# Kernel optimization log

Measured on AMD Instinct MI355X. Metric: run time of the kernel, lower is better.

The kernel has to match this reference:

```python
import jax, jax.numpy as jnp
import numpy as np

N_LAYER, N_HEAD, D_PARAM = 4, 8, 63
BATCH, SEQ, D_FULL = 16, 2048, D_PARAM + 1
VAR = 0.02


def setup_inputs() -> dict:
    key = jax.random.key(0)
    kz, kp = jax.random.split(key)
    Z = jax.random.normal(kz, (BATCH, SEQ, D_FULL), dtype=jnp.float32)
    allparam = VAR * jax.random.normal(kp, (N_LAYER, N_HEAD, 2, D_PARAM, D_PARAM), dtype=jnp.float32)
    return {"Z": Z, "allparam": allparam}


def _augment(P, Q, d_full):
    # P_full: P in top-left block, bottom-right corner = 1, rest zeros.
    dp = P.shape[0]
    P_full = jnp.zeros((d_full, d_full), P.dtype).at[:dp, :dp].set(P).at[dp, dp].set(1.0)
    # Q_full: Q in top-left block, rest zeros (bottom-right corner stays 0).
    Q_full = jnp.zeros((d_full, d_full), Q.dtype).at[:dp, :dp].set(Q)
    return P_full, Q_full


def _attention(P, Q, Z):
    B, N, d = Z.shape
    P_full, Q_full = _augment(P, Q, d)
    # attn[b,n,m] = Z[b,n,:] @ Q_full @ Z[b,m,:]
    attn = jnp.einsum('BNi,ij,BMj->BNM', Z, Q_full, Z)
    key = jnp.einsum('ij,BNj->BNi', P_full, Z)
    # A = eye(N) with A[N-1,N-1] = 0  => zero out last token of key before aggregation.
    key = key.at[:, N - 1, :].set(0.0)
    out = jnp.einsum('BNM,BMi->BNi', attn, key)
    return out / (N - 1)


def reference(Z, allparam):
    n_layer, n_head = allparam.shape[0], allparam.shape[1]
    for i in range(n_layer):
        Zi = Z
        residues = jnp.zeros_like(Z)
        for j in range(n_head):
            residues = residues + _attention(allparam[i, j, 0], allparam[i, j, 1], Zi)
        Z = Zi + residues
    return Z
```

## Files before the change

kernel.cpp:

```cpp
#include <hip/hip_runtime.h>
#include <hip/hip_bf16.h>

constexpr int NL = 4;
constexpr int NH = 8;
constexpr int DP = 63;
constexpr int D  = 64;
constexpr int B  = 16;
constexpr int S  = 2048;
constexpr int CHUNKS = 16;
constexpr int ROWS_PER_CHUNK = S / CHUNKS;

__global__ __launch_bounds__(256) void kA(const float* __restrict__ Z,
                                          float* __restrict__ Gp) {
    const int b = blockIdx.x;
    const int c = blockIdx.y;
    __shared__ float lz[64][64];
    const int t   = threadIdx.x;
    const int col = t & 63;
    const int rb  = t >> 6;

    float acc[16];
#pragma unroll
    for (int k = 0; k < 16; ++k) acc[k] = 0.f;

    const int rowbase = c * ROWS_PER_CHUNK;
    for (int sub = 0; sub < ROWS_PER_CHUNK / 64; ++sub) {
#pragma unroll
        for (int k = 0; k < 16; ++k) {
            int row  = rb + 4 * k;
            int grow = rowbase + sub * 64 + row;
            float v  = Z[((size_t)b * S + grow) * D + col];
            if (grow == S - 1) v = 0.f;
            lz[row][col] = v;
        }
        __syncthreads();
        for (int m = 0; m < 64; ++m) {
            float zr = lz[m][col];
#pragma unroll
            for (int k = 0; k < 16; ++k)
                acc[k] += lz[m][rb + 4 * k] * zr;
        }
        __syncthreads();
    }
    float* outp = Gp + ((size_t)(c * B + b)) * (D * D);
#pragma unroll
    for (int k = 0; k < 16; ++k)
        outp[(rb + 4 * k) * D + col] = acc[k];
}

__global__ __launch_bounds__(256) void kB(const float* __restrict__ Gp,
                                          const float* __restrict__ allparam,
                                          float* __restrict__ H, int layer) {
    const int b = blockIdx.x;
    const int j = blockIdx.y;
    __shared__ float G[64 * 64];
    __shared__ float PfT[64 * 64];
    __shared__ float Qf[64 * 64];
    __shared__ float T[64 * 64];

    const int t   = threadIdx.x;
    const int col = t & 63;
    const int rb  = t >> 6;

#pragma unroll
    for (int k = 0; k < 16; ++k) {
        int e = t + 256 * k;
        float s = 0.f;
        for (int c2 = 0; c2 < CHUNKS; ++c2)
            s += Gp[((size_t)(c2 * B + b)) * (D * D) + e];
        G[e] = s;
    }

    const float* P = allparam + ((size_t)((layer * NH + j) * 2 + 0)) * (DP * DP);
    const float* Q = allparam + ((size_t)((layer * NH + j) * 2 + 1)) * (DP * DP);
#pragma unroll
    for (int k = 0; k < 16; ++k) {
        int e = t + 256 * k;
        int r = e >> 6, i = e & 63;
        float pv = 0.f;
        if (r < DP && i < DP) pv = P[i * DP + r];
        if (r == DP && i == DP) pv = 1.f;
        PfT[e] = pv;
        int p = r, q = i;
        Qf[e] = (p < DP && q < DP) ? Q[p * DP + q] : 0.f;
    }
    __syncthreads();

    {
        float acc[16];
#pragma unroll
        for (int k = 0; k < 16; ++k) acc[k] = 0.f;
        for (int r = 0; r < 64; ++r) {
            float pv = PfT[r * 64 + col];
#pragma unroll
            for (int k = 0; k < 16; ++k)
                acc[k] += G[(rb + 4 * k) * 64 + r] * pv;
        }
#pragma unroll
        for (int k = 0; k < 16; ++k)
            T[(rb + 4 * k) * 64 + col] = acc[k];
    }
    __syncthreads();

    {
        const float inv = 1.0f / (float)(S - 1);
        float acc[16];
#pragma unroll
        for (int k = 0; k < 16; ++k) acc[k] = 0.f;
        for (int q = 0; q < 64; ++q) {
            float tv = T[q * 64 + col];
#pragma unroll
            for (int k = 0; k < 16; ++k)
                acc[k] += Qf[(rb + 4 * k) * 64 + q] * tv;
        }
        float* Hout = H + ((size_t)(b * NH + j)) * (D * D);
#pragma unroll
        for (int k = 0; k < 16; ++k)
            Hout[(rb + 4 * k) * 64 + col] = acc[k] * inv;
    }
}

__global__ __launch_bounds__(256) void kB2(const float* __restrict__ H,
                                           float* __restrict__ W) {
    const int b = blockIdx.x;
    const int t = threadIdx.x;
#pragma unroll
    for (int k = 0; k < 16; ++k) {
        int e = t + 256 * k;
        float s = ((e >> 6) == (e & 63)) ? 1.f : 0.f;
        for (int j = 0; j < NH; ++j)
            s += H[((size_t)(b * NH + j)) * (D * D) + e];
        W[(size_t)b * (D * D) + e] = s;
    }
}

__global__ __launch_bounds__(256) void kC(const float* Zin,
                                          const float* __restrict__ W,
                                          float* Zout) {
    const int b    = blockIdx.x;
    const int tile = blockIdx.y;
    __shared__ float lz[64][64];
    __shared__ float lw[64][64];
    const int t   = threadIdx.x;
    const int col = t & 63;
    const int rb  = t >> 6;

#pragma unroll
    for (int k = 0; k < 16; ++k) {
        int e = t + 256 * k;
        lw[e >> 6][e & 63] = W[(size_t)b * (D * D) + e];
    }
    const size_t zbase = ((size_t)b * S + (size_t)tile * 64) * D;
#pragma unroll
    for (int k = 0; k < 16; ++k) {
        int row = rb + 4 * k;
        lz[row][col] = Zin[zbase + (size_t)row * D + col];
    }
    __syncthreads();

    float acc[16];
#pragma unroll
    for (int k = 0; k < 16; ++k) acc[k] = 0.f;
    for (int p = 0; p < 64; ++p) {
        float wv = lw[p][col];
#pragma unroll
        for (int k = 0; k < 16; ++k)
            acc[k] += lz[rb + 4 * k][p] * wv;
    }
#pragma unroll
    for (int k = 0; k < 16; ++k) {
        int row = rb + 4 * k;
        Zout[zbase + (size_t)row * D + col] = acc[k];
    }
}

extern "C" void kernel_launch(void* const* d_in, const int* in_sizes, int n_in,
                              void* d_out, int out_size, void* d_ws, size_t ws_size,
                              hipStream_t stream) {
    const float* Z        = (const float*)d_in[0];
    const float* allparam = (const float*)d_in[1];
    float* out = (float*)d_out;

    float* Gp = (float*)d_ws;
    float* H  = Gp + (size_t)CHUNKS * B * (D * D);
    float* W  = H + (size_t)B * NH * (D * D);

    for (int layer = 0; layer < NL; ++layer) {
        const float* src = (layer == 0) ? Z : (const float*)out;
        kA <<<dim3(B, CHUNKS), 256, 0, stream>>>(src, Gp);
        kB <<<dim3(B, NH),     256, 0, stream>>>(Gp, allparam, H, layer);
        kB2<<<B,               256, 0, stream>>>(H, W);
        kC <<<dim3(B, S / 64), 256, 0, stream>>>(src, W, out);
    }
}
```

Measured before the change: 225.2 us.

## Fuse next-layer Gram into Z update, register-tile GEMMs, atomic head accumulation

Replaces the per-layer four-kernel pipeline with a first Gram kernel plus, per layer, a reduce kernel, a weight kernel and an update kernel. The update kernel also computes the next layer's partial Gram from the freshly computed tile, so Z is not re-read. The GEMMs now use 8x8 and 4x4 register tiles with float4 loads and XOR-swizzled shared memory. Head contributions go into W through atomicAdd instead of a separate sum kernel. Atomics make the float summation order nondeterministic, and the larger shared-memory use may lower occupancy.

New measurement: 210.5 us. 6.6% less time.

```diff
diff --git a/kernel.cpp b/kernel.cpp
--- a/kernel.cpp
+++ b/kernel.cpp
@@ -1,177 +1,213 @@
 #include <hip/hip_runtime.h>
-#include <hip/hip_bf16.h>
-
-constexpr int NL = 4;
-constexpr int NH = 8;
-constexpr int DP = 63;
-constexpr int D  = 64;
-constexpr int B  = 16;
-constexpr int S  = 2048;
-constexpr int CHUNKS = 16;
-constexpr int ROWS_PER_CHUNK = S / CHUNKS;
-
-__global__ __launch_bounds__(256) void kA(const float* __restrict__ Z,
-                                          float* __restrict__ Gp) {
-    const int b = blockIdx.x;
-    const int c = blockIdx.y;
-    __shared__ float lz[64][64];
-    const int t   = threadIdx.x;
-    const int col = t & 63;
-    const int rb  = t >> 6;
-
-    float acc[16];
-#pragma unroll
-    for (int k = 0; k < 16; ++k) acc[k] = 0.f;
-
-    const int rowbase = c * ROWS_PER_CHUNK;
-    for (int sub = 0; sub < ROWS_PER_CHUNK / 64; ++sub) {
-#pragma unroll
-        for (int k = 0; k < 16; ++k) {
-            int row  = rb + 4 * k;
-            int grow = rowbase + sub * 64 + row;
-            float v  = Z[((size_t)b * S + grow) * D + col];
-            if (grow == S - 1) v = 0.f;
-            lz[row][col] = v;
+
+constexpr int NH = 8, DP = 63, D = 64, B = 16, S = 2048;
+constexpr int TILE = 128, NTILE = 16;
+constexpr float INVS = 1.0f / 2047.0f;
+
+__device__ __forceinline__ void gram_reduce_store(const float* ZN, float4* sm4,
+                                                  float* __restrict__ gp, int t) {
+    const int w = t >> 6, l = t & 63, qy = l >> 3, rx = l & 7;
+    float g[8][8];
+#pragma unroll
+    for (int a = 0; a < 8; ++a)
+#pragma unroll
+        for (int bb = 0; bb < 8; ++bb) g[a][bb] = 0.f;
+
+#pragma unroll 4
+    for (int mi = 0; mi < 32; ++mi) {
+        const int m = 32 * w + mi;
+        const int f = (m >> 3) & 15;
+        const float* rowp = &ZN[m * 64];
+        float4 a0 = *(const float4*)&rowp[4 * (qy ^ f)];
+        float4 a1 = *(const float4*)&rowp[4 * ((qy + 8) ^ f)];
+        float4 b0 = *(const float4*)&rowp[4 * (rx ^ f)];
+        float4 b1 = *(const float4*)&rowp[4 * ((rx + 8) ^ f)];
+        float A[8]  = {a0.x, a0.y, a0.z, a0.w, a1.x, a1.y, a1.z, a1.w};
+        float Bv[8] = {b0.x, b0.y, b0.z, b0.w, b1.x, b1.y, b1.z, b1.w};
+#pragma unroll
+        for (int a = 0; a < 8; ++a)
+#pragma unroll
+            for (int bb = 0; bb < 8; ++bb) g[a][bb] += A[a] * Bv[bb];
+    }
+    __syncthreads();
+
+    float* part = (float*)(sm4 + w * 1024);
+#pragma unroll
+    for (int a = 0; a < 8; ++a) {
+        const int q = 4 * qy + (a & 3) + 32 * (a >> 2);
+        *(float4*)&part[q * 64 + 4 * rx]      = make_float4(g[a][0], g[a][1], g[a][2], g[a][3]);
+        *(float4*)&part[q * 64 + 32 + 4 * rx] = make_float4(g[a][4], g[a][5], g[a][6], g[a][7]);
+    }
+    __syncthreads();
+
+    float4* gp4 = (float4*)gp;
+#pragma unroll
+    for (int k = 0; k < 4; ++k) {
+        const int e4 = t + 256 * k;
+        float4 s0 = sm4[e4], s1 = sm4[1024 + e4], s2 = sm4[2048 + e4], s3 = sm4[3072 + e4];
+        gp4[e4] = make_float4(s0.x + s1.x + s2.x + s3.x, s0.y + s1.y + s2.y + s3.y,
+                              s0.z + s1.z + s2.z + s3.z, s0.w + s1.w + s2.w + s3.w);
+    }
+}
+
+__global__ __launch_bounds__(256) void kGram0(const float* __restrict__ Z,
+                                              float* __restrict__ Gp) {
+    __shared__ float4 sm4[5120];
+    float* ZN = (float*)(sm4 + 3072);
+    const int b = blockIdx.x, tile = blockIdx.y, t = threadIdx.x;
+#pragma unroll
+    for (int k = 0; k < 8; ++k) {
+        const int row = (t >> 4) + 16 * k, c4 = t & 15;
+        const int grow = tile * TILE + row;
+        float4 v = *(const float4*)&Z[((size_t)b * S + grow) * D + 4 * c4];
+        if (grow == S - 1) v = make_float4(0.f, 0.f, 0.f, 0.f);
+        *(float4*)&ZN[row * 64 + 4 * (c4 ^ ((row >> 3) & 15))] = v;
+    }
+    __syncthreads();
+    gram_reduce_store(ZN, sm4, Gp + ((size_t)(b * 16 + tile)) * 4096, t);
+}
+
+__global__ __launch_bounds__(256) void kRed(const float* __restrict__ Gp,
+                                            float* __restrict__ G,
+                                            float* __restrict__ W) {
+    const int b = blockIdx.x, s = blockIdx.y, t = threadIdx.x;
+    const int e = s * 256 + t;
+    float sum = 0.f;
+#pragma unroll 4
+    for (int p = 0; p < 16; ++p) sum += Gp[((size_t)(b * 16 + p)) * 4096 + e];
+    G[(size_t)b * 4096 + e] = sum;
+    W[(size_t)b * 4096 + e] = ((e >> 6) == (e & 63)) ? 1.f : 0.f;
+}
+
+__global__ __launch_bounds__(128) void kW(const float* __restrict__ G,
+                                          const float* __restrict__ params,
+                                          float* __restrict__ W) {
+    __shared__ float4 sm4[(4096 + 2048 + 4096 + 2048) / 4];
+    float* Gs = (float*)sm4;
+    float* Pt = Gs + 4096;
+    float* Qt = Pt + 2048;
+    float* T  = Qt + 4096;
+    const int b = blockIdx.x, j = blockIdx.y, s = blockIdx.z, t = threadIdx.x;
+    const int ty = t >> 3, tx = t & 7;
+    const float* P = params + (size_t)(j * 2 + 0) * (DP * DP);
+    const float* Q = params + (size_t)(j * 2 + 1) * (DP * DP);
+
+#pragma unroll
+    for (int k = 0; k < 8; ++k)
+        ((float4*)Gs)[t + 128 * k] = ((const float4*)(G + (size_t)b * 4096))[t + 128 * k];
+#pragma unroll
+    for (int k = 0; k < 16; ++k) {
+        const int r = t & 63, ii = (t >> 6) + 2 * k;
+        const int i = 32 * s + ii;
+        float v = 0.f;
+        if (r < DP && i < DP) v = P[(size_t)i * DP + r];
+        else if (r == DP && i == DP) v = 1.f;
+        Pt[r * 32 + 4 * ((ii >> 2) ^ (r & 7)) + (ii & 3)] = v;
+    }
+#pragma unroll
+    for (int k = 0; k < 32; ++k) {
+        const int q = t & 63, p = (t >> 6) + 2 * k;
+        const float v = (p < DP && q < DP) ? Q[(size_t)p * DP + q] : 0.f;
+        Qt[q * 64 + 4 * ((p >> 2) ^ (q & 15)) + (p & 3)] = v;
+    }
+    __syncthreads();
+
+    float acc[4][4] = {};
+#pragma unroll 4
+    for (int r = 0; r < 64; ++r) {
+        float4 av = *(const float4*)&Gs[r * 64 + 4 * ty];
+        float4 bv = *(const float4*)&Pt[r * 32 + 4 * (tx ^ (r & 7))];
+        float A[4] = {av.x, av.y, av.z, av.w}, Bb[4] = {bv.x, bv.y, bv.z, bv.w};
+#pragma unroll
+        for (int a = 0; a < 4; ++a)
+#pragma unroll
+            for (int c = 0; c < 4; ++c) acc[a][c] += A[a] * Bb[c];
+    }
+#pragma unroll
+    for (int a = 0; a < 4; ++a)
+        *(float4*)&T[(4 * ty + a) * 32 + 4 * tx] =
+            make_float4(acc[a][0], acc[a][1], acc[a][2], acc[a][3]);
+    __syncthreads();
+
+    float acc2[4][4] = {};
+#pragma unroll 4
+    for (int q = 0; q < 64; ++q) {
+        float4 av = *(const float4*)&Qt[q * 64 + 4 * (ty ^ (q & 15))];
+        float4 bv = *(const float4*)&T[q * 32 + 4 * tx];
+        float A[4] = {av.x, av.y, av.z, av.w}, Bb[4] = {bv.x, bv.y, bv.z, bv.w};
+#pragma unroll
+        for (int a = 0; a < 4; ++a)
+#pragma unroll
+            for (int c = 0; c < 4; ++c) acc2[a][c] += A[a] * Bb[c];
+    }
+    float* Wb = W + (size_t)b * 4096;
+#pragma unroll
+    for (int a = 0; a < 4; ++a)
+#pragma unroll
+        for (int c = 0; c < 4; ++c)
+            atomicAdd(&Wb[(4 * ty + a) * 64 + 32 * s + 4 * tx + c], acc2[a][c] * INVS);
+}
+
+__global__ __launch_bounds__(256) void kCA(const float* __restrict__ src,
+                                           const float* __restrict__ W,
+                                           float* __restrict__ out,
+                                           float* __restrict__ Gp, int do_gram) {
+    __shared__ float4 sm4[5120];
+    float* ZT = (float*)sm4;
+    float* Ws = (float*)(sm4 + 2048);
+    float* ZN = (float*)(sm4 + 3072);
+    const int b = blockIdx.x, tile = blockIdx.y, t = threadIdx.x;
+    const int ny = t & 15, ix = t >> 4;
+    const size_t zbase = ((size_t)b * S + tile * TILE) * D;
+
+#pragma unroll
+    for (int k = 0; k < 4; ++k)
+        sm4[2048 + t + 256 * k] = ((const float4*)(W + (size_t)b * 4096))[t + 256 * k];
+#pragma unroll
+    for (int k = 0; k < 8; ++k) {
+        const int row = (t >> 4) + 16 * k, c4 = t & 15;
+        float4 v = *(const float4*)&src[zbase + (size_t)row * D + 4 * c4];
+        float vv[4] = {v.x, v.y, v.z, v.w};
+#pragma unroll
+        for (int c = 0; c < 4; ++c) {
+            const int p = 4 * c4 + c;
+            ZT[p * 128 + 4 * ((row >> 2) ^ c4) + (row & 3)] = vv[c];
         }
-        __syncthreads();
-        for (int m = 0; m < 64; ++m) {
-            float zr = lz[m][col];
-#pragma unroll
-            for (int k = 0; k < 16; ++k)
-                acc[k] += lz[m][rb + 4 * k] * zr;
-        }
-        __syncthreads();
-    }
-    float* outp = Gp + ((size_t)(c * B + b)) * (D * D);
-#pragma unroll
-    for (int k = 0; k < 16; ++k)
-        outp[(rb + 4 * k) * D + col] = acc[k];
-}
-
-__global__ __launch_bounds__(256) void kB(const float* __restrict__ Gp,
-                                          const float* __restrict__ allparam,
-                                          float* __restrict__ H, int layer) {
-    const int b = blockIdx.x;
-    const int j = blockIdx.y;
-    __shared__ float G[64 * 64];
-    __shared__ float PfT[64 * 64];
-    __shared__ float Qf[64 * 64];
-    __shared__ float T[64 * 64];
-
-    const int t   = threadIdx.x;
-    const int col = t & 63;
-    const int rb  = t >> 6;
-
-#pragma unroll
-    for (int k = 0; k < 16; ++k) {
-        int e = t + 256 * k;
-        float s = 0.f;
-        for (int c2 = 0; c2 < CHUNKS; ++c2)
-            s += Gp[((size_t)(c2 * B + b)) * (D * D) + e];
-        G[e] = s;
-    }
-
-    const float* P = allparam + ((size_t)((layer * NH + j) * 2 + 0)) * (DP * DP);
-    const float* Q = allparam + ((size_t)((layer * NH + j) * 2 + 1)) * (DP * DP);
-#pragma unroll
-    for (int k = 0; k < 16; ++k) {
-        int e = t + 256 * k;
-        int r = e >> 6, i = e & 63;
-        float pv = 0.f;
-        if (r < DP && i < DP) pv = P[i * DP + r];
-        if (r == DP && i == DP) pv = 1.f;
-        PfT[e] = pv;
-        int p = r, q = i;
-        Qf[e] = (p < DP && q < DP) ? Q[p * DP + q] : 0.f;
-    }
-    __syncthreads();
-
-    {
-        float acc[16];
-#pragma unroll
-        for (int k = 0; k < 16; ++k) acc[k] = 0.f;
-        for (int r = 0; r < 64; ++r) {
-            float pv = PfT[r * 64 + col];
-#pragma unroll
-            for (int k = 0; k < 16; ++k)
-                acc[k] += G[(rb + 4 * k) * 64 + r] * pv;
-        }
-#pragma unroll
-        for (int k = 0; k < 16; ++k)
-            T[(rb + 4 * k) * 64 + col] = acc[k];
-    }
-    __syncthreads();
-
-    {
-        const float inv = 1.0f / (float)(S - 1);
-        float acc[16];
-#pragma unroll
-        for (int k = 0; k < 16; ++k) acc[k] = 0.f;
-        for (int q = 0; q < 64; ++q) {
-            float tv = T[q * 64 + col];
-#pragma unroll
-            for (int k = 0; k < 16; ++k)
-                acc[k] += Qf[(rb + 4 * k) * 64 + q] * tv;
-        }
-        float* Hout = H + ((size_t)(b * NH + j)) * (D * D);
-#pragma unroll
-        for (int k = 0; k < 16; ++k)
-            Hout[(rb + 4 * k) * 64 + col] = acc[k] * inv;
-    }
-}
-
-__global__ __launch_bounds__(256) void kB2(const float* __restrict__ H,
-                                           float* __restrict__ W) {
-    const int b = blockIdx.x;
-    const int t = threadIdx.x;
-#pragma unroll
-    for (int k = 0; k < 16; ++k) {
-        int e = t + 256 * k;
-        float s = ((e >> 6) == (e & 63)) ? 1.f : 0.f;
-        for (int j = 0; j < NH; ++j)
-            s += H[((size_t)(b * NH + j)) * (D * D) + e];
-        W[(size_t)b * (D * D) + e] = s;
-    }
-}
-
-__global__ __launch_bounds__(256) void kC(const float* Zin,
-                                          const float* __restrict__ W,
-                                          float* Zout) {
-    const int b    = blockIdx.x;
-    const int tile = blockIdx.y;
-    __shared__ float lz[64][64];
-    __shared__ float lw[64][64];
-    const int t   = threadIdx.x;
-    const int col = t & 63;
-    const int rb  = t >> 6;
-
-#pragma unroll
-    for (int k = 0; k < 16; ++k) {
-        int e = t + 256 * k;
-        lw[e >> 6][e & 63] = W[(size_t)b * (D * D) + e];
-    }
-    const size_t zbase = ((size_t)b * S + (size_t)tile * 64) * D;
-#pragma unroll
-    for (int k = 0; k < 16; ++k) {
-        int row = rb + 4 * k;
-        lz[row][col] = Zin[zbase + (size_t)row * D + col];
-    }
-    __syncthreads();
-
-    float acc[16];
-#pragma unroll
-    for (int k = 0; k < 16; ++k) acc[k] = 0.f;
+    }
+    __syncthreads();
+
+    float acc[8][4] = {};
+#pragma unroll 4
     for (int p = 0; p < 64; ++p) {
-        float wv = lw[p][col];
-#pragma unroll
-        for (int k = 0; k < 16; ++k)
-            acc[k] += lz[rb + 4 * k][p] * wv;
-    }
-#pragma unroll
-    for (int k = 0; k < 16; ++k) {
-        int row = rb + 4 * k;
-        Zout[zbase + (size_t)row * D + col] = acc[k];
-    }
+        const int f = p >> 2;
+        const float* zp = &ZT[p * 128];
+        float4 a0 = *(const float4*)&zp[4 * (ny ^ f)];
+        float4 a1 = *(const float4*)&zp[4 * ((ny + 16) ^ f)];
+        float4 wv = *(const float4*)&Ws[p * 64 + 4 * ix];
+        float A[8] = {a0.x, a0.y, a0.z, a0.w, a1.x, a1.y, a1.z, a1.w};
+        float Wv[4] = {wv.x, wv.y, wv.z, wv.w};
+#pragma unroll
+        for (int a = 0; a < 8; ++a)
+#pragma unroll
+            for (int c = 0; c < 4; ++c) acc[a][c] += A[a] * Wv[c];
+    }
+#pragma unroll
+    for (int a = 0; a < 8; ++a) {
+        const int n = 4 * ny + (a & 3) + 64 * (a >> 2);
+        *(float4*)&out[zbase + (size_t)n * D + 4 * ix] =
+            make_float4(acc[a][0], acc[a][1], acc[a][2], acc[a][3]);
+    }
+    if (!do_gram) return;
+
+#pragma unroll
+    for (int a = 0; a < 8; ++a) {
+        const int n = 4 * ny + (a & 3) + 64 * (a >> 2);
+        float4 vv = make_float4(acc[a][0], acc[a][1], acc[a][2], acc[a][3]);
+        if (tile == NTILE - 1 && n == TILE - 1) vv = make_float4(0.f, 0.f, 0.f, 0.f);
+        *(float4*)&ZN[n * 64 + 4 * (ix ^ ((n >> 3) & 15))] = vv;
+    }
+    __syncthreads();
+    gram_reduce_store(ZN, sm4, Gp + ((size_t)(b * 16 + tile)) * 4096, t);
 }
 
 extern "C" void kernel_launch(void* const* d_in, const int* in_sizes, int n_in,
@@ -182,14 +218,15 @@
     float* out = (float*)d_out;
 
     float* Gp = (float*)d_ws;
-    float* H  = Gp + (size_t)CHUNKS * B * (D * D);
-    float* W  = H + (size_t)B * NH * (D * D);
-
-    for (int layer = 0; layer < NL; ++layer) {
+    float* G  = Gp + (size_t)B * 16 * 4096;
+    float* W  = G + (size_t)B * 4096;
+
+    kGram0<<<dim3(B, NTILE), 256, 0, stream>>>(Z, Gp);
+    for (int layer = 0; layer < 4; ++layer) {
         const float* src = (layer == 0) ? Z : (const float*)out;
-        kA <<<dim3(B, CHUNKS), 256, 0, stream>>>(src, Gp);
-        kB <<<dim3(B, NH),     256, 0, stream>>>(Gp, allparam, H, layer);
-        kB2<<<B,               256, 0, stream>>>(H, W);
-        kC <<<dim3(B, S / 64), 256, 0, stream>>>(src, W, out);
-    }
-}
+        const float* params = allparam + (size_t)layer * NH * 2 * DP * DP;
+        kRed<<<dim3(B, 16), 256, 0, stream>>>(Gp, G, W);
+        kW<<<dim3(B, NH, 2), 128, 0, stream>>>(G, params, W);
+        kCA<<<dim3(B, NTILE), 256, 0, stream>>>(src, W, out, Gp, layer < 3 ? 1 : 0);
+    }
+}
```
